# Kernel tuning notes

Hardware: AMD Instinct MI355X
Metric: run time of the kernel (lower is better)

## Reference

```python
import jax, jax.numpy as jnp
import numpy as np

B, S, D = 32, 4096, 512

def setup_inputs() -> dict:
    key = jax.random.key(0)
    ks = jax.random.split(key, 5)
    scale = 1.0 / np.sqrt(D)
    return {
        "query": jax.random.normal(ks[0], (B, D), jnp.float32),
        "values": jax.random.normal(ks[1], (B, S, D), jnp.float32),
        "W1": jax.random.normal(ks[2], (D, D), jnp.float32) * scale,
        "b1": jnp.zeros((D,), jnp.float32),
        "W2": jax.random.normal(ks[3], (D, D), jnp.float32) * scale,
        "b2": jnp.zeros((D,), jnp.float32),
        "V": jax.random.normal(ks[4], (D, 1), jnp.float32) * scale,
        "bv": jnp.zeros((1,), jnp.float32),
    }

def reference(query, values, W1, b1, W2, b2, V, bv):
    # query: [B, D], values: [B, S, D]
    q_proj = query @ W1 + b1                      # [B, D]
    v_proj = jnp.einsum('bsd,de->bse', values, W2) + b2  # [B, S, D]
    hidden = jnp.tanh(q_proj[:, None, :] + v_proj)       # [B, S, D]
    score = jnp.einsum('bsd,de->bse', hidden, V) + bv    # [B, S, 1]
    attn = jax.nn.softmax(score, axis=1)                 # softmax over seq axis
    context = jnp.sum(attn * values, axis=1)             # [B, D]
    return (context, attn)
```

## Files before the change

kernel.cpp:

```cpp
#include <hip/hip_runtime.h>
#include <hip/hip_bf16.h>
#include <stdint.h>

#define NB 32
#define NS 4096
#define ND 512

typedef __attribute__((ext_vector_type(8))) short short8;
typedef __attribute__((ext_vector_type(4))) float floatx4;
typedef __attribute__((ext_vector_type(4))) unsigned int uint4v;

__device__ __forceinline__ short f2bf(float f) {
    unsigned int u = __builtin_bit_cast(unsigned int, f);
    return (short)((u + 0x8000u) >> 16);
}

__device__ __forceinline__ unsigned int cvt_pk_bf16(float lo, float hi) {
    unsigned int r;
    asm("v_cvt_pk_bf16_f32 %0, %1, %2" : "=v"(r) : "v"(lo), "v"(hi));
    return r;
}

__device__ __forceinline__ float fast_tanh(float x) {
    float e = __expf(2.0f * x);
    return 1.0f - 2.0f * __builtin_amdgcn_rcpf(e + 1.0f);
}

__global__ void __launch_bounds__(256) qproj_kernel(
    const float* __restrict__ query, const float* __restrict__ W1,
    const float* __restrict__ b1, const float* __restrict__ b2,
    float* __restrict__ qb) {
    const int b  = blockIdx.x;
    const int es = blockIdx.y;
    const int t  = threadIdx.x;
    const int col = t & 63, kc = t >> 6;
    __shared__ float q[ND];
    __shared__ float red[256];
    q[t] = query[b * ND + t];
    q[t + 256] = query[b * ND + t + 256];
    __syncthreads();
    float acc = 0.f;
    const float* wp = W1 + (size_t)(kc * 128) * ND + es * 64 + col;
    const float* qp = q + kc * 128;
#pragma unroll 8
    for (int k = 0; k < 128; k++)
        acc += qp[k] * wp[(size_t)k * ND];
    red[t] = acc;
    __syncthreads();
    if (t < 64) {
        float s = red[t] + red[t + 64] + red[t + 128] + red[t + 192];
        int e = es * 64 + t;
        qb[b * ND + e] = s + b1[e] + b2[e];
    }
}

__global__ void __launch_bounds__(256) w2t_kernel(
    const float* __restrict__ W2, unsigned short* __restrict__ W2Tt) {
    int g = blockIdx.x * 256 + threadIdx.x;
    int nt = g >> 14;
    int ks = (g >> 10) & 15;
    int kq = (g >> 8) & 3;
    int n  = g & 255;
    int e  = nt * 256 + n;
    int k0 = ks * 32 + kq * 8;
    short8 v;
#pragma unroll
    for (int j = 0; j < 8; j++)
        v[j] = f2bf(W2[(size_t)(k0 + j) * ND + e]);
    *(short8*)&W2Tt[(size_t)g * 8] = v;
}

__global__ void __launch_bounds__(256, 3) scores_kernel(
    const float* __restrict__ values, const unsigned short* __restrict__ W2Tt,
    const float* __restrict__ qb, const float* __restrict__ V,
    float* __restrict__ pscores) {
    const int nt = blockIdx.x;
    const int st = blockIdx.y;
    const int b  = blockIdx.z;
    const int n0 = nt * 256, s0 = st * 64;

    __shared__ __align__(16) unsigned short sA[2][2048];
    __shared__ float sQb[256];
    __shared__ float sV[256];
    __shared__ float sRed[4][64];

    const int tid  = threadIdx.x;
    const int lane = tid & 63;
    const int wave = tid >> 6;
    const int mr = lane & 15;
    const int q  = lane >> 4;

    sQb[tid] = qb[b * ND + n0 + tid];
    sV[tid]  = V[n0 + tid];

    floatx4 acc[4][4] = {};

    const int arow = tid >> 2;
    const int ac   = tid & 3;
    const int ardo = arow * 32 + ((ac ^ ((tid >> 3) & 3)) * 8);
    const float* ag = values + ((size_t)b * NS + s0 + arow) * ND + ac * 8;

    const int afo = (q ^ ((mr >> 1) & 3)) * 8;

    const unsigned short* bp = W2Tt + (size_t)nt * 16 * 8192 + (q * 256 + wave * 64 + mr) * 8;

    float4 p0 = *(const float4*)(ag);
    float4 p1 = *(const float4*)(ag + 4);
    short8 bq[3][4];
#pragma unroll
    for (int j = 0; j < 4; j++)
        bq[0][j] = *(const short8*)(bp + j * 128);
#pragma unroll
    for (int j = 0; j < 4; j++)
        bq[1][j] = *(const short8*)(bp + 8192 + j * 128);
    float4 aq[4][2];
    aq[1][0] = *(const float4*)(ag + 32);  aq[1][1] = *(const float4*)(ag + 36);
    aq[2][0] = *(const float4*)(ag + 64);  aq[2][1] = *(const float4*)(ag + 68);
    aq[3][0] = *(const float4*)(ag + 96);  aq[3][1] = *(const float4*)(ag + 100);
    {
        uint4v w;
        w.x = cvt_pk_bf16(p0.x, p0.y); w.y = cvt_pk_bf16(p0.z, p0.w);
        w.z = cvt_pk_bf16(p1.x, p1.y); w.w = cvt_pk_bf16(p1.z, p1.w);
        *(uint4v*)&sA[0][ardo] = w;
    }
    asm volatile("s_waitcnt lgkmcnt(0)" ::: "memory");
    __builtin_amdgcn_s_barrier();
    __builtin_amdgcn_sched_barrier(0);

#pragma unroll
    for (int ks = 0; ks < 16; ks++) {
        const int cur = ks & 1, nxt = cur ^ 1;

        short8 af[4];
#pragma unroll
        for (int i = 0; i < 4; i++)
            af[i] = *(const short8*)&sA[cur][(i * 16 + mr) * 32 + afo];

        if (ks < 15) {
            const float4 a0 = aq[(ks + 1) & 3][0], a1 = aq[(ks + 1) & 3][1];
            uint4v w;
            w.x = cvt_pk_bf16(a0.x, a0.y); w.y = cvt_pk_bf16(a0.z, a0.w);
            w.z = cvt_pk_bf16(a1.x, a1.y); w.w = cvt_pk_bf16(a1.z, a1.w);
            *(uint4v*)&sA[nxt][ardo] = w;
        }
        __builtin_amdgcn_sched_barrier(0);

        if (ks < 14) {
            const unsigned short* bsrc = bp + (size_t)(ks + 2) * 8192;
#pragma unroll
            for (int j = 0; j < 4; j++)
                bq[(ks + 2) % 3][j] = *(const short8*)(bsrc + j * 128);
        }
        __builtin_amdgcn_sched_barrier(0);
        if (ks < 12) {
            aq[(ks + 4) & 3][0] = *(const float4*)(ag + (ks + 4) * 32);
            aq[(ks + 4) & 3][1] = *(const float4*)(ag + (ks + 4) * 32 + 4);
        }
        __builtin_amdgcn_sched_barrier(0);

        __builtin_amdgcn_s_setprio(1);
#pragma unroll
        for (int i = 0; i < 4; i++)
#pragma unroll
            for (int j = 0; j < 4; j++)
                acc[i][j] = __builtin_amdgcn_mfma_f32_16x16x32_bf16(af[i], bq[ks % 3][j], acc[i][j], 0, 0, 0);
        __builtin_amdgcn_s_setprio(0);

        asm volatile("s_waitcnt lgkmcnt(0)" ::: "memory");
        __builtin_amdgcn_s_barrier();
        __builtin_amdgcn_sched_barrier(0);
    }

    float vcoef[4], qadd[4];
#pragma unroll
    for (int j = 0; j < 4; j++) {
        int col = wave * 64 + j * 16 + mr;
        vcoef[j] = sV[col];
        qadd[j]  = sQb[col];
    }

#pragma unroll
    for (int i = 0; i < 4; i++) {
#pragma unroll
        for (int r = 0; r < 4; r++) {
            float p = 0.f;
#pragma unroll
            for (int j = 0; j < 4; j++)
                p += fast_tanh(acc[i][j][r] + qadd[j]) * vcoef[j];
            p += __shfl_xor(p, 1);
            p += __shfl_xor(p, 2);
            p += __shfl_xor(p, 4);
            p += __shfl_xor(p, 8);
            if (mr == 0) sRed[wave][i * 16 + q * 4 + r] = p;
        }
    }
    __syncthreads();
    if (tid < 64) {
        float s = sRed[0][tid] + sRed[1][tid] + sRed[2][tid] + sRed[3][tid];
        pscores[((size_t)nt * NB + b) * NS + s0 + tid] = s;
    }
}

__global__ void __launch_bounds__(256) softmax_kernel(
    const float* __restrict__ pscores, float* __restrict__ attn) {
    int b = blockIdx.x;
    int t = threadIdx.x;
    __shared__ float red[4];
    __shared__ float bcast[2];
    const float* sc0 = pscores + (size_t)b * NS;
    const float* sc1 = pscores + (size_t)(NB + b) * NS;
    float v[16];
    float m = -1e30f;
#pragma unroll
    for (int i = 0; i < 16; i++) {
        v[i] = sc0[t + i * 256] + sc1[t + i * 256];
        m = fmaxf(m, v[i]);
    }
    for (int o = 32; o; o >>= 1) m = fmaxf(m, __shfl_xor(m, o));
    if ((t & 63) == 0) red[t >> 6] = m;
    __syncthreads();
    if (t == 0) bcast[0] = fmaxf(fmaxf(red[0], red[1]), fmaxf(red[2], red[3]));
    __syncthreads();
    m = bcast[0];
    float sum = 0.f;
#pragma unroll
    for (int i = 0; i < 16; i++) { v[i] = __expf(v[i] - m); sum += v[i]; }
    for (int o = 32; o; o >>= 1) sum += __shfl_xor(sum, o);
    if ((t & 63) == 0) red[t >> 6] = sum;
    __syncthreads();
    if (t == 0) bcast[1] = red[0] + red[1] + red[2] + red[3];
    __syncthreads();
    float inv = 1.0f / bcast[1];
    float* ao = attn + (size_t)b * NS;
#pragma unroll
    for (int i = 0; i < 16; i++) ao[t + i * 256] = v[i] * inv;
}

__global__ void __launch_bounds__(256) context_partial_kernel(
    const float* __restrict__ values, const float* __restrict__ attn,
    float* __restrict__ pctx) {
    int sc = blockIdx.x;
    int b  = blockIdx.y;
    int t  = threadIdx.x;
    __shared__ float sAttn[128];
    if (t < 128) sAttn[t] = attn[(size_t)b * NS + sc * 128 + t];
    __syncthreads();
    int d = t * 2;
    const float2* vp = (const float2*)(values + ((size_t)b * NS + sc * 128) * ND + d);
    float ax = 0.f, ay = 0.f;
#pragma unroll 8
    for (int s = 0; s < 128; s++) {
        float a = sAttn[s];
        float2 v = vp[(size_t)s * 256];
        ax += a * v.x; ay += a * v.y;
    }
    pctx[((size_t)sc * 32 + b) * ND + d]     = ax;
    pctx[((size_t)sc * 32 + b) * ND + d + 1] = ay;
}

__global__ void __launch_bounds__(256) context_reduce_kernel(
    const float* __restrict__ pctx, float* __restrict__ ctx) {
    int i = blockIdx.x * 256 + threadIdx.x;
    float s = 0.f;
#pragma unroll
    for (int p = 0; p < 32; p++) s += pctx[(size_t)p * (32 * ND) + i];
    ctx[i] = s;
}

extern "C" void kernel_launch(void* const* d_in, const int* in_sizes, int n_in,
                              void* d_out, int out_size, void* d_ws, size_t ws_size,
                              hipStream_t stream) {
    const float* query  = (const float*)d_in[0];
    const float* values = (const float*)d_in[1];
    const float* W1     = (const float*)d_in[2];
    const float* b1     = (const float*)d_in[3];
    const float* W2     = (const float*)d_in[4];
    const float* b2     = (const float*)d_in[5];
    const float* V      = (const float*)d_in[6];

    float* ctx_out  = (float*)d_out;
    float* attn_out = (float*)d_out + NB * ND;

    char* ws = (char*)d_ws;
    float*          qb      = (float*)ws;
    unsigned short* W2Tt    = (unsigned short*)(ws + (64 << 10));
    float*          pscores = (float*)(ws + (576 << 10));
    float*          pctx    = (float*)(ws + (1600 << 10));

    qproj_kernel<<<dim3(NB, 8), 256, 0, stream>>>(query, W1, b1, b2, qb);
    w2t_kernel<<<128, 256, 0, stream>>>(W2, W2Tt);
    scores_kernel<<<dim3(2, 64, 32), 256, 0, stream>>>(values, W2Tt, qb, V, pscores);
    softmax_kernel<<<NB, 256, 0, stream>>>(pscores, attn_out);
    context_partial_kernel<<<dim3(32, 32), 256, 0, stream>>>(values, attn_out, pctx);
    context_reduce_kernel<<<64, 256, 0, stream>>>(pctx, ctx_out);
}
```

Baseline: 469.9 us.

## Compute both output-column halves per block, staging the full values tile in LDS once

The scores kernel now handles all 512 output columns in one block instead of splitting them across two blocks. The whole 64x512 values tile is converted to bf16 into shared memory up front, which halves the global reads and conversions of values. The main loop then runs 32 k-steps without per-step barriers, and the tanh/V reduction is applied after each 256-column half. The softmax no longer sums two partial score arrays. In exchange the block uses 64KB of LDS and occupancy drops to 2 blocks per CU, with half as many blocks in the grid, and the tile load is no longer overlapped with MFMA work.

```diff
diff --git a/kernel.cpp b/kernel.cpp
--- a/kernel.cpp
+++ b/kernel.cpp
@@ -70,18 +70,17 @@
     *(short8*)&W2Tt[(size_t)g * 8] = v;
 }
 
-__global__ void __launch_bounds__(256, 3) scores_kernel(
+__global__ void __launch_bounds__(256, 2) scores_kernel(
     const float* __restrict__ values, const unsigned short* __restrict__ W2Tt,
     const float* __restrict__ qb, const float* __restrict__ V,
     float* __restrict__ pscores) {
-    const int nt = blockIdx.x;
-    const int st = blockIdx.y;
-    const int b  = blockIdx.z;
-    const int n0 = nt * 256, s0 = st * 64;
-
-    __shared__ __align__(16) unsigned short sA[2][2048];
-    __shared__ float sQb[256];
-    __shared__ float sV[256];
+    const int st = blockIdx.x;
+    const int b  = blockIdx.y;
+    const int s0 = st * 64;
+
+    __shared__ __align__(16) unsigned short sA[16][2048];
+    __shared__ float sQb[ND];
+    __shared__ float sV[ND];
     __shared__ float sRed[4][64];
 
     const int tid  = threadIdx.x;
@@ -90,114 +89,121 @@
     const int mr = lane & 15;
     const int q  = lane >> 4;
 
-    sQb[tid] = qb[b * ND + n0 + tid];
-    sV[tid]  = V[n0 + tid];
-
-    floatx4 acc[4][4] = {};
+    sQb[tid] = qb[b * ND + tid];
+    sQb[tid + 256] = qb[b * ND + tid + 256];
+    sV[tid]  = V[tid];
+    sV[tid + 256] = V[tid + 256];
 
     const int arow = tid >> 2;
     const int ac   = tid & 3;
     const int ardo = arow * 32 + ((ac ^ ((tid >> 3) & 3)) * 8);
     const float* ag = values + ((size_t)b * NS + s0 + arow) * ND + ac * 8;
 
-    const int afo = (q ^ ((mr >> 1) & 3)) * 8;
-
-    const unsigned short* bp = W2Tt + (size_t)nt * 16 * 8192 + (q * 256 + wave * 64 + mr) * 8;
-
-    float4 p0 = *(const float4*)(ag);
-    float4 p1 = *(const float4*)(ag + 4);
-    short8 bq[3][4];
-#pragma unroll
-    for (int j = 0; j < 4; j++)
-        bq[0][j] = *(const short8*)(bp + j * 128);
-#pragma unroll
-    for (int j = 0; j < 4; j++)
-        bq[1][j] = *(const short8*)(bp + 8192 + j * 128);
-    float4 aq[4][2];
-    aq[1][0] = *(const float4*)(ag + 32);  aq[1][1] = *(const float4*)(ag + 36);
-    aq[2][0] = *(const float4*)(ag + 64);  aq[2][1] = *(const float4*)(ag + 68);
-    aq[3][0] = *(const float4*)(ag + 96);  aq[3][1] = *(const float4*)(ag + 100);
     {
-        uint4v w;
-        w.x = cvt_pk_bf16(p0.x, p0.y); w.y = cvt_pk_bf16(p0.z, p0.w);
-        w.z = cvt_pk_bf16(p1.x, p1.y); w.w = cvt_pk_bf16(p1.z, p1.w);
-        *(uint4v*)&sA[0][ardo] = w;
-    }
-    asm volatile("s_waitcnt lgkmcnt(0)" ::: "memory");
-    __builtin_amdgcn_s_barrier();
-    __builtin_amdgcn_sched_barrier(0);
-
-#pragma unroll
-    for (int ks = 0; ks < 16; ks++) {
-        const int cur = ks & 1, nxt = cur ^ 1;
-
-        short8 af[4];
-#pragma unroll
-        for (int i = 0; i < 4; i++)
-            af[i] = *(const short8*)&sA[cur][(i * 16 + mr) * 32 + afo];
-
-        if (ks < 15) {
-            const float4 a0 = aq[(ks + 1) & 3][0], a1 = aq[(ks + 1) & 3][1];
+        float4 aq[4][2];
+#pragma unroll
+        for (int u = 0; u < 4; u++) {
+            aq[u][0] = *(const float4*)(ag + u * 32);
+            aq[u][1] = *(const float4*)(ag + u * 32 + 4);
+        }
+#pragma unroll
+        for (int ks = 0; ks < 16; ks++) {
+            const float4 a0 = aq[ks & 3][0], a1 = aq[ks & 3][1];
+            if (ks < 12) {
+                aq[ks & 3][0] = *(const float4*)(ag + (ks + 4) * 32);
+                aq[ks & 3][1] = *(const float4*)(ag + (ks + 4) * 32 + 4);
+            }
             uint4v w;
             w.x = cvt_pk_bf16(a0.x, a0.y); w.y = cvt_pk_bf16(a0.z, a0.w);
             w.z = cvt_pk_bf16(a1.x, a1.y); w.w = cvt_pk_bf16(a1.z, a1.w);
-            *(uint4v*)&sA[nxt][ardo] = w;
-        }
-        __builtin_amdgcn_sched_barrier(0);
-
-        if (ks < 14) {
-            const unsigned short* bsrc = bp + (size_t)(ks + 2) * 8192;
+            *(uint4v*)&sA[ks][ardo] = w;
+        }
+    }
+    __syncthreads();
+
+    const int afo = (q ^ ((mr >> 1) & 3)) * 8;
+    const unsigned short* bp = W2Tt + (q * 256 + wave * 64 + mr) * 8;
+
+    floatx4 acc[4][4] = {};
+    float p[4][4] = {};
+    short8 af[2][4], bq[2][4];
+
+#pragma unroll
+    for (int i = 0; i < 4; i++)
+        af[0][i] = *(const short8*)&sA[0][(i * 16 + mr) * 32 + afo];
+#pragma unroll
+    for (int j = 0; j < 4; j++)
+        bq[0][j] = *(const short8*)(bp + j * 128);
+
+#pragma unroll
+    for (int hk = 0; hk < 32; hk++) {
+        const int cur = hk & 1, nxt = cur ^ 1;
+        const int ks = hk & 15;
+
+        if (hk < 31) {
+            const unsigned short* bsrc = bp + (size_t)(hk + 1) * 8192;
 #pragma unroll
             for (int j = 0; j < 4; j++)
-                bq[(ks + 2) % 3][j] = *(const short8*)(bsrc + j * 128);
-        }
-        __builtin_amdgcn_sched_barrier(0);
-        if (ks < 12) {
-            aq[(ks + 4) & 3][0] = *(const float4*)(ag + (ks + 4) * 32);
-            aq[(ks + 4) & 3][1] = *(const float4*)(ag + (ks + 4) * 32 + 4);
-        }
-        __builtin_amdgcn_sched_barrier(0);
+                bq[nxt][j] = *(const short8*)(bsrc + j * 128);
+#pragma unroll
+            for (int i = 0; i < 4; i++)
+                af[nxt][i] = *(const short8*)&sA[(hk + 1) & 15][(i * 16 + mr) * 32 + afo];
+        }
 
         __builtin_amdgcn_s_setprio(1);
 #pragma unroll
         for (int i = 0; i < 4; i++)
 #pragma unroll
             for (int j = 0; j < 4; j++)
-                acc[i][j] = __builtin_amdgcn_mfma_f32_16x16x32_bf16(af[i], bq[ks % 3][j], acc[i][j], 0, 0, 0);
+                acc[i][j] = __builtin_amdgcn_mfma_f32_16x16x32_bf16(af[cur][i], bq[cur][j], acc[i][j], 0, 0, 0);
         __builtin_amdgcn_s_setprio(0);
 
-        asm volatile("s_waitcnt lgkmcnt(0)" ::: "memory");
-        __builtin_amdgcn_s_barrier();
-        __builtin_amdgcn_sched_barrier(0);
-    }
-
-    float vcoef[4], qadd[4];
-#pragma unroll
-    for (int j = 0; j < 4; j++) {
-        int col = wave * 64 + j * 16 + mr;
-        vcoef[j] = sV[col];
-        qadd[j]  = sQb[col];
+        if (ks == 15) {
+            const int h = hk >> 4;
+            float vcoef[4], qadd[4];
+#pragma unroll
+            for (int j = 0; j < 4; j++) {
+                int col = h * 256 + wave * 64 + j * 16 + mr;
+                vcoef[j] = sV[col];
+                qadd[j]  = sQb[col];
+            }
+#pragma unroll
+            for (int i = 0; i < 4; i++)
+#pragma unroll
+                for (int r = 0; r < 4; r++) {
+                    float s = 0.f;
+#pragma unroll
+                    for (int j = 0; j < 4; j++)
+                        s += fast_tanh(acc[i][j][r] + qadd[j]) * vcoef[j];
+                    p[i][r] += s;
+                    if (hk < 31) acc[i][0][r] = 0.f;
+                }
+            if (hk < 31) {
+#pragma unroll
+                for (int i = 0; i < 4; i++)
+#pragma unroll
+                    for (int j = 1; j < 4; j++)
+                        acc[i][j] = floatx4{0.f, 0.f, 0.f, 0.f};
+            }
+        }
     }
 
 #pragma unroll
     for (int i = 0; i < 4; i++) {
 #pragma unroll
         for (int r = 0; r < 4; r++) {
-            float p = 0.f;
-#pragma unroll
-            for (int j = 0; j < 4; j++)
-                p += fast_tanh(acc[i][j][r] + qadd[j]) * vcoef[j];
-            p += __shfl_xor(p, 1);
-            p += __shfl_xor(p, 2);
-            p += __shfl_xor(p, 4);
-            p += __shfl_xor(p, 8);
-            if (mr == 0) sRed[wave][i * 16 + q * 4 + r] = p;
+            float v = p[i][r];
+            v += __shfl_xor(v, 1);
+            v += __shfl_xor(v, 2);
+            v += __shfl_xor(v, 4);
+            v += __shfl_xor(v, 8);
+            if (mr == 0) sRed[wave][i * 16 + q * 4 + r] = v;
         }
     }
     __syncthreads();
     if (tid < 64) {
         float s = sRed[0][tid] + sRed[1][tid] + sRed[2][tid] + sRed[3][tid];
-        pscores[((size_t)nt * NB + b) * NS + s0 + tid] = s;
+        pscores[(size_t)b * NS + s0 + tid] = s;
     }
 }
 
@@ -207,15 +213,11 @@
     int t = threadIdx.x;
     __shared__ float red[4];
     __shared__ float bcast[2];
-    const float* sc0 = pscores + (size_t)b * NS;
-    const float* sc1 = pscores + (size_t)(NB + b) * NS;
+    const float* sc = pscores + (size_t)b * NS;
     float v[16];
     float m = -1e30f;
 #pragma unroll
-    for (int i = 0; i < 16; i++) {
-        v[i] = sc0[t + i * 256] + sc1[t + i * 256];
-        m = fmaxf(m, v[i]);
-    }
+    for (int i = 0; i < 16; i++) { v[i] = sc[t + i * 256]; m = fmaxf(m, v[i]); }
     for (int o = 32; o; o >>= 1) m = fmaxf(m, __shfl_xor(m, o));
     if ((t & 63) == 0) red[t >> 6] = m;
     __syncthreads();
@@ -285,11 +287,11 @@
     float*          qb      = (float*)ws;
     unsigned short* W2Tt    = (unsigned short*)(ws + (64 << 10));
     float*          pscores = (float*)(ws + (576 << 10));
-    float*          pctx    = (float*)(ws + (1600 << 10));
+    float*          pctx    = (float*)(ws + (1088 << 10));
 
     qproj_kernel<<<dim3(NB, 8), 256, 0, stream>>>(query, W1, b1, b2, qb);
     w2t_kernel<<<128, 256, 0, stream>>>(W2, W2Tt);
-    scores_kernel<<<dim3(2, 64, 32), 256, 0, stream>>>(values, W2Tt, qb, V, pscores);
+    scores_kernel<<<dim3(64, 32), 256, 0, stream>>>(values, W2Tt, qb, V, pscores);
     softmax_kernel<<<NB, 256, 0, stream>>>(pscores, attn_out);
     context_partial_kernel<<<dim3(32, 32), 256, 0, stream>>>(values, attn_out, pctx);
     context_reduce_kernel<<<64, 256, 0, stream>>>(pctx, ctx_out);
```

Result: no change. 477.2 us (+1.6%).
